# Optimization experiments

Measured on AMD Instinct MI355X. Metric: run time of the kernel, lower is better.

Reference implementation:

```python
import jax, jax.numpy as jnp
import numpy as np

SEQ_FEAT = 1024   # sequence_length (input feature dim of Linear layers)
ATT = 512         # attention_size
P_DROP = 0.2
B, T = 8, 2048


def setup_inputs() -> dict:
    key = jax.random.key(0)
    k1, k2, k3, k4, k5 = jax.random.split(key, 5)
    s = 1.0 / np.sqrt(SEQ_FEAT)
    x = jax.random.normal(k1, (B, T, SEQ_FEAT), dtype=jnp.float32)
    Wq = jax.random.normal(k2, (ATT, SEQ_FEAT), dtype=jnp.float32) * s
    Wk = jax.random.normal(k3, (ATT, SEQ_FEAT), dtype=jnp.float32) * s
    Wv = jax.random.normal(k4, (SEQ_FEAT, SEQ_FEAT), dtype=jnp.float32) * s
    drop_mask = jax.random.uniform(k5, (B, T, T)) >= P_DROP  # keep where True
    return {"x": x, "Wq": Wq, "Wk": Wk, "Wv": Wv, "drop_mask": drop_mask}


def reference(x, Wq, Wk, Wv, drop_mask):
    # Linear (no bias): y = x @ W.T, torch Linear weight is [out, in]
    q = jnp.einsum('btf,af->bta', x, Wq)          # [B,T,ATT]
    k = jnp.einsum('btf,af->bta', x, Wk)          # [B,T,ATT]
    v = jnp.einsum('btf,gf->btg', x, Wv)          # [B,T,SEQ_FEAT]
    scores = jnp.einsum('bta,bsa->bts', q, k) / jnp.sqrt(jnp.float32(ATT))
    attn = jax.nn.softmax(scores, axis=-1)
    # dropout (training=True in F.dropout): scale kept entries by 1/(1-p)
    attn = jnp.where(drop_mask, attn / (1.0 - P_DROP), 0.0)
    out = jnp.einsum('bts,bsg->btg', attn, v)     # [B,T,SEQ_FEAT]
    return out
```

## Files before the change

### kernel.cpp

```cpp
#include <hip/hip_runtime.h>

typedef unsigned short u16;
typedef _Float16 h16;
typedef __attribute__((ext_vector_type(4))) float f32x4;
typedef __attribute__((ext_vector_type(8))) _Float16 h16x8;
typedef __attribute__((ext_vector_type(4))) _Float16 h16x4;
typedef __attribute__((ext_vector_type(4))) int i32x4;

__global__ __launch_bounds__(256) void k_cast_all(
    const float* __restrict__ x, const float* __restrict__ wq,
    const float* __restrict__ wk, const float* __restrict__ wv,
    const int* __restrict__ mask,
    h16* __restrict__ xf, h16* __restrict__ wqk, h16* __restrict__ wvf,
    unsigned* __restrict__ bits) {
  const int bid = blockIdx.x;
  if (bid < 2048) {
    size_t base = ((size_t)bid * 256 + threadIdx.x) * 64;
    const i32x4* m4 = (const i32x4*)(mask + base);
    i32x4 v[16];
#pragma unroll
    for (int j = 0; j < 16; ++j) v[j] = m4[j];
    unsigned long long bb = 0ull;
#pragma unroll
    for (int j = 0; j < 16; ++j) {
      unsigned nib = (unsigned)(v[j][0] != 0) | ((unsigned)(v[j][1] != 0) << 1) |
                     ((unsigned)(v[j][2] != 0) << 2) | ((unsigned)(v[j][3] != 0) << 3);
      bb |= (unsigned long long)nib << (j * 4);
    }
    ((unsigned long long*)bits)[base >> 6] = bb;
    return;
  }
  const int cb = bid - 2048;
  const float* src;
  h16* dst;
  size_t qb;
  if (cb < 1024) { src = x;  dst = xf;           qb = (size_t)cb * 4096; }
  else if (cb < 1056) { src = wq; dst = wqk;          qb = (size_t)(cb - 1024) * 4096; }
  else if (cb < 1088) { src = wk; dst = wqk + 524288; qb = (size_t)(cb - 1056) * 4096; }
  else { src = wv; dst = wvf;          qb = (size_t)(cb - 1088) * 4096; }
  f32x4 v[16];
#pragma unroll
  for (int j = 0; j < 16; ++j)
    v[j] = ((const f32x4*)src)[qb + j * 256 + threadIdx.x];
#pragma unroll
  for (int j = 0; j < 16; ++j) {
    h16x4 o;
#pragma unroll
    for (int e = 0; e < 4; ++e) o[e] = (h16)v[j][e];
    ((h16x4*)dst)[qb + j * 256 + threadIdx.x] = o;
  }
}

__device__ __forceinline__ void gl16(const u16* src, u16* dst) {
  __builtin_amdgcn_global_load_lds(
      (const __attribute__((address_space(1))) unsigned*)src,
      (__attribute__((address_space(3))) unsigned*)dst, 16, 0, 0);
}

__device__ __forceinline__ void swz_block(int& bn, int& bm, int& bz) {
  int gx = gridDim.x, gy = gridDim.y;
  int flat = blockIdx.x + gx * (blockIdx.y + gy * blockIdx.z);
  int nwg = gx * gy * (int)gridDim.z;
  int q = nwg >> 3;
  int id = (flat & 7) * q + (flat >> 3);
  bn = id % gx;
  id /= gx;
  bm = id % gy;
  bz = id / gy;
}

template <int NT, int EPI>
__global__ __launch_bounds__(512, 2) void k_gemm(
    const u16* __restrict__ A, int lda, long long aZ,
    const u16* __restrict__ B, int ldb, long long bZ,
    void* __restrict__ Cp, int ldc, long long cZ, float scale,
    const unsigned* __restrict__ bits, float* __restrict__ dnm) {
  __shared__ u16 lds[3 * 16384];
  int bn, bm, bz;
  swz_block(bn, bm, bz);
  const int tid = threadIdx.x;
  const int lane = tid & 63;
  const int wr = (tid >> 6) >> 2, wc = (tid >> 6) & 3;
  const u16* A0 = A + (size_t)bz * aZ + (size_t)bm * 256 * lda;
  const u16* B0 = B + (size_t)bz * bZ + (size_t)bn * 256 * ldb;

  const int lc = ((tid & 3) ^ ((tid >> 3) & 3)) << 3;
  const int r0s = tid >> 2;

  auto STAGE = [&](int t, int slot) {
    if (t >= NT) return;
    int kk = t << 5;
    u16* dst = &lds[0] + slot * 16384;
    gl16(A0 + (size_t)r0s * lda + kk + lc, dst + tid * 8);
    gl16(A0 + (size_t)(r0s + 128) * lda + kk + lc, dst + 4096 + tid * 8);
    gl16(B0 + (size_t)r0s * ldb + kk + lc, dst + 8192 + tid * 8);
    gl16(B0 + (size_t)(r0s + 128) * ldb + kk + lc, dst + 12288 + tid * 8);
  };

  const int fr = lane & 15;
  const int pch = (((lane >> 4) ^ ((fr >> 1) & 3)) << 3);
  const int abase = (wr * 128 + fr) * 32 + pch;
  const int bbase = 8192 + (wc * 64 + fr) * 32 + pch;

  f32x4 acc[8][4] = {};

  STAGE(0, 0);
  STAGE(1, 1);
  asm volatile("s_waitcnt vmcnt(4)" ::: "memory");
  __builtin_amdgcn_s_barrier();
  asm volatile("" ::: "memory");

  int slot = 0, pslot = 2;
#pragma unroll 1
  for (int T = 0; T < NT; ++T) {
    const int sb = slot * 16384;
    h16x8 av[8], bv[4];
#pragma unroll
    for (int n = 0; n < 4; ++n) bv[n] = *(const h16x8*)&lds[sb + bbase + n * 512];
#pragma unroll
    for (int m = 0; m < 8; ++m) av[m] = *(const h16x8*)&lds[sb + abase + m * 512];
    STAGE(T + 2, pslot);
    __builtin_amdgcn_s_setprio(1);
#pragma unroll
    for (int m = 0; m < 8; ++m)
#pragma unroll
      for (int n = 0; n < 4; ++n)
        acc[m][n] = __builtin_amdgcn_mfma_f32_16x16x32_f16(av[m], bv[n], acc[m][n], 0, 0, 0);
    __builtin_amdgcn_s_setprio(0);
    if (T < NT - 2)
      asm volatile("s_waitcnt vmcnt(4)" ::: "memory");
    else
      asm volatile("s_waitcnt vmcnt(0)" ::: "memory");
    __builtin_amdgcn_s_barrier();
    asm volatile("" ::: "memory");
    slot = (slot == 2) ? 0 : slot + 1;
    pslot = (pslot == 2) ? 0 : pslot + 1;
  }

  const size_t zc = (size_t)bz * cZ;

  if constexpr (EPI == 0) {
#pragma unroll
    for (int m = 0; m < 8; ++m)
#pragma unroll
      for (int n = 0; n < 4; ++n)
#pragma unroll
        for (int r = 0; r < 4; ++r) {
          int row = bm * 256 + wr * 128 + m * 16 + (lane >> 4) * 4 + r;
          int col = bn * 256 + wc * 64 + n * 16 + fr;
          ((h16*)Cp)[zc + (size_t)row * ldc + col] = (h16)acc[m][n][r];
        }
  } else if constexpr (EPI == 5) {
    float* red = (float*)&lds[0];
    const unsigned* bw = bits + (size_t)bz * 2048 * 64 + bn * 8 + wc * 2;
#pragma unroll
    for (int m = 0; m < 8; ++m)
#pragma unroll
      for (int r = 0; r < 4; ++r) {
        int rowl = wr * 128 + m * 16 + (lane >> 4) * 4 + r;
        int row = bm * 256 + rowl;
        unsigned w0 = bw[(size_t)row * 64];
        unsigned w1 = bw[(size_t)row * 64 + 1];
        float rs = 0.f;
#pragma unroll
        for (int n = 0; n < 4; ++n) {
          int col = bn * 256 + wc * 64 + n * 16 + fr;
          float e = __expf(acc[m][n][r] * scale);
          rs += e;
          unsigned wv_ = (n < 2) ? w0 : w1;
          bool keep = (wv_ >> ((n & 1) * 16 + fr)) & 1u;
          ((h16*)Cp)[zc + (size_t)row * ldc + col] = keep ? (h16)e : (h16)0.f;
        }
        rs += __shfl_xor(rs, 1);
        rs += __shfl_xor(rs, 2);
        rs += __shfl_xor(rs, 4);
        rs += __shfl_xor(rs, 8);
        if ((lane & 15) == 0) red[rowl * 4 + wc] = rs;
      }
    __syncthreads();
    if (tid < 256) {
      float d = red[tid * 4] + red[tid * 4 + 1] + red[tid * 4 + 2] + red[tid * 4 + 3];
      dnm[(size_t)bn * 16384 + (size_t)bz * 2048 + bm * 256 + tid] = d;
    }
  } else {
    float* dinv = (float*)&lds[0];
    if (tid < 256) {
      float d = 0.f;
#pragma unroll
      for (int j = 0; j < 8; ++j)
        d += dnm[(size_t)j * 16384 + (size_t)bz * 2048 + bm * 256 + tid];
      dinv[tid] = 1.0f / (0.8f * d);
    }
    __syncthreads();
#pragma unroll
    for (int m = 0; m < 8; ++m)
#pragma unroll
      for (int n = 0; n < 4; ++n)
#pragma unroll
        for (int r = 0; r < 4; ++r) {
          int rowl = wr * 128 + m * 16 + (lane >> 4) * 4 + r;
          int row = bm * 256 + rowl;
          int col = bn * 256 + wc * 64 + n * 16 + fr;
          ((float*)Cp)[zc + (size_t)row * ldc + col] = acc[m][n][r] * dinv[rowl];
        }
  }
}

extern "C" void kernel_launch(void* const* d_in, const int* in_sizes, int n_in,
                              void* d_out, int out_size, void* d_ws, size_t ws_size,
                              hipStream_t stream) {
  const float* x  = (const float*)d_in[0];
  const float* Wq = (const float*)d_in[1];
  const float* Wk = (const float*)d_in[2];
  const float* Wv = (const float*)d_in[3];
  const int* mask = (const int*)d_in[4];
  float* out = (float*)d_out;

  u16* ws = (u16*)d_ws;
  h16* xf  = (h16*)ws;
  h16* Wqk = (h16*)(ws + 16777216);
  h16* Wvf = (h16*)(ws + 17825792);
  h16* qk  = (h16*)(ws + 18874368);
  h16* vvt = (h16*)(ws + 35651584);
  h16* Pb  = (h16*)(ws + 52428864);
  float* dnm = (float*)(ws + 85983296);
  unsigned* bits = (unsigned*)(ws + 86245440);

  k_cast_all<<<3200, 256, 0, stream>>>(x, Wq, Wk, Wv, mask, xf, Wqk, Wvf, bits);

  dim3 gqk(4, 64, 1);
  k_gemm<32, 0><<<gqk, 512, 0, stream>>>((const u16*)xf, 1024, 0,
                                         (const u16*)Wqk, 1024, 0, qk, 1024, 0, 0.f,
                                         (const unsigned*)0, (float*)0);

  dim3 gvt(64, 4, 1);
  k_gemm<32, 0><<<gvt, 512, 0, stream>>>((const u16*)Wvf, 1024, 0,
                                         (const u16*)xf, 1024, 0, vvt, 16384, 0, 0.f,
                                         (const unsigned*)0, (float*)0);

  const float scale = 0.044194173824159216f;
  dim3 gs(8, 8, 8);
  k_gemm<16, 5><<<gs, 512, 0, stream>>>((const u16*)qk, 1024, 2097152,
                                        (const u16*)(qk + 512), 1024, 2097152,
                                        Pb, 2048, 4194304, scale, bits, dnm);

  dim3 gpv(4, 8, 8);
  k_gemm<64, 6><<<gpv, 512, 0, stream>>>((const u16*)Pb, 2048, 4194304,
                                         (const u16*)vvt, 16384, 2048,
                                         out, 1024, 2097152, 1.0f,
                                         (const unsigned*)0, dnm);

  (void)in_sizes; (void)n_in; (void)out_size; (void)ws_size;
}
```

Before: 276.4 us.

## Fuse dropout-mask bit packing into the scores GEMM epilogue

Removes the separate mask-to-bitfield pass from the cast kernel. The scores GEMM epilogue now reads its 256x256 tile of the int32 mask directly, packs it into an LDS bit table with wave ballots, and looks up keep bits from LDS. This drops one full write and read of the packed bit buffer and a kernel phase. In exchange the epilogue does extra global loads and an extra barrier while holding GEMM registers, which may stall the tail of the scores kernel.

```diff
diff --git a/kernel.cpp b/kernel.cpp
--- a/kernel.cpp
+++ b/kernel.cpp
@@ -10,27 +10,8 @@
 __global__ __launch_bounds__(256) void k_cast_all(
     const float* __restrict__ x, const float* __restrict__ wq,
     const float* __restrict__ wk, const float* __restrict__ wv,
-    const int* __restrict__ mask,
-    h16* __restrict__ xf, h16* __restrict__ wqk, h16* __restrict__ wvf,
-    unsigned* __restrict__ bits) {
-  const int bid = blockIdx.x;
-  if (bid < 2048) {
-    size_t base = ((size_t)bid * 256 + threadIdx.x) * 64;
-    const i32x4* m4 = (const i32x4*)(mask + base);
-    i32x4 v[16];
-#pragma unroll
-    for (int j = 0; j < 16; ++j) v[j] = m4[j];
-    unsigned long long bb = 0ull;
-#pragma unroll
-    for (int j = 0; j < 16; ++j) {
-      unsigned nib = (unsigned)(v[j][0] != 0) | ((unsigned)(v[j][1] != 0) << 1) |
-                     ((unsigned)(v[j][2] != 0) << 2) | ((unsigned)(v[j][3] != 0) << 3);
-      bb |= (unsigned long long)nib << (j * 4);
-    }
-    ((unsigned long long*)bits)[base >> 6] = bb;
-    return;
-  }
-  const int cb = bid - 2048;
+    h16* __restrict__ xf, h16* __restrict__ wqk, h16* __restrict__ wvf) {
+  const int cb = blockIdx.x;
   const float* src;
   h16* dst;
   size_t qb;
@@ -74,7 +55,7 @@
     const u16* __restrict__ A, int lda, long long aZ,
     const u16* __restrict__ B, int ldb, long long bZ,
     void* __restrict__ Cp, int ldc, long long cZ, float scale,
-    const unsigned* __restrict__ bits, float* __restrict__ dnm) {
+    const int* __restrict__ maskp, float* __restrict__ dnm) {
   __shared__ u16 lds[3 * 16384];
   int bn, bm, bz;
   swz_block(bn, bm, bz);
@@ -151,24 +132,49 @@
           ((h16*)Cp)[zc + (size_t)row * ldc + col] = (h16)acc[m][n][r];
         }
   } else if constexpr (EPI == 5) {
-    float* red = (float*)&lds[0];
-    const unsigned* bw = bits + (size_t)bz * 2048 * 64 + bn * 8 + wc * 2;
+    unsigned long long* tbl = (unsigned long long*)&lds[0];
+    float* red = (float*)&lds[4096];
+    {
+      const int w = tid >> 6;
+      const int* mrow0 = maskp + ((size_t)bz * 2048 + bm * 256) * 2048 + bn * 256;
+#pragma unroll 1
+      for (int i = 0; i < 4; ++i) {
+        i32x4 mv[8];
+#pragma unroll
+        for (int j = 0; j < 8; ++j)
+          mv[j] = *(const i32x4*)(mrow0 + (size_t)(i * 64 + j * 8 + w) * 2048 + lane * 4);
+#pragma unroll
+        for (int j = 0; j < 8; ++j) {
+          int row = i * 64 + j * 8 + w;
+          unsigned long long b0 = __ballot(mv[j][0] != 0);
+          unsigned long long b1 = __ballot(mv[j][1] != 0);
+          unsigned long long b2 = __ballot(mv[j][2] != 0);
+          unsigned long long b3 = __ballot(mv[j][3] != 0);
+          if (lane == 0) {
+            tbl[row * 4 + 0] = b0;
+            tbl[row * 4 + 1] = b1;
+            tbl[row * 4 + 2] = b2;
+            tbl[row * 4 + 3] = b3;
+          }
+        }
+      }
+    }
+    __syncthreads();
+    const int bsh = wc * 16 + (fr >> 2);
 #pragma unroll
     for (int m = 0; m < 8; ++m)
 #pragma unroll
       for (int r = 0; r < 4; ++r) {
         int rowl = wr * 128 + m * 16 + (lane >> 4) * 4 + r;
         int row = bm * 256 + rowl;
-        unsigned w0 = bw[(size_t)row * 64];
-        unsigned w1 = bw[(size_t)row * 64 + 1];
+        unsigned long long wb = tbl[rowl * 4 + (fr & 3)];
         float rs = 0.f;
 #pragma unroll
         for (int n = 0; n < 4; ++n) {
           int col = bn * 256 + wc * 64 + n * 16 + fr;
           float e = __expf(acc[m][n][r] * scale);
           rs += e;
-          unsigned wv_ = (n < 2) ? w0 : w1;
-          bool keep = (wv_ >> ((n & 1) * 16 + fr)) & 1u;
+          bool keep = (wb >> (bsh + n * 4)) & 1ull;
           ((h16*)Cp)[zc + (size_t)row * ldc + col] = keep ? (h16)e : (h16)0.f;
         }
         rs += __shfl_xor(rs, 1);
@@ -224,31 +230,30 @@
   h16* vvt = (h16*)(ws + 35651584);
   h16* Pb  = (h16*)(ws + 52428864);
   float* dnm = (float*)(ws + 85983296);
-  unsigned* bits = (unsigned*)(ws + 86245440);
-
-  k_cast_all<<<3200, 256, 0, stream>>>(x, Wq, Wk, Wv, mask, xf, Wqk, Wvf, bits);
+
+  k_cast_all<<<1152, 256, 0, stream>>>(x, Wq, Wk, Wv, xf, Wqk, Wvf);
 
   dim3 gqk(4, 64, 1);
   k_gemm<32, 0><<<gqk, 512, 0, stream>>>((const u16*)xf, 1024, 0,
                                          (const u16*)Wqk, 1024, 0, qk, 1024, 0, 0.f,
-                                         (const unsigned*)0, (float*)0);
+                                         (const int*)0, (float*)0);
 
   dim3 gvt(64, 4, 1);
   k_gemm<32, 0><<<gvt, 512, 0, stream>>>((const u16*)Wvf, 1024, 0,
                                          (const u16*)xf, 1024, 0, vvt, 16384, 0, 0.f,
-                                         (const unsigned*)0, (float*)0);
+                                         (const int*)0, (float*)0);
 
   const float scale = 0.044194173824159216f;
   dim3 gs(8, 8, 8);
   k_gemm<16, 5><<<gs, 512, 0, stream>>>((const u16*)qk, 1024, 2097152,
                                         (const u16*)(qk + 512), 1024, 2097152,
-                                        Pb, 2048, 4194304, scale, bits, dnm);
+                                        Pb, 2048, 4194304, scale, mask, dnm);
 
   dim3 gpv(4, 8, 8);
   k_gemm<64, 6><<<gpv, 512, 0, stream>>>((const u16*)Pb, 2048, 4194304,
                                          (const u16*)vvt, 16384, 2048,
                                          out, 1024, 2097152, 1.0f,
-                                         (const unsigned*)0, dnm);
+                                         (const int*)0, dnm);
 
   (void)in_sizes; (void)n_in; (void)out_size; (void)ws_size;
 }
```

Result: faster. 258.0 us (-6.7%).
